# Kernel tuning notes

Measured on AMD Instinct MI355X. Metric: run time of the kernel, lower is better.

Reference implementation:

```python
import jax, jax.numpy as jnp
import numpy as np

H = 8        # num_heads
D = 768      # d_model
DH = D // H  # d_head = 96


def setup_inputs() -> dict:
    key = jax.random.key(0)
    ks = jax.random.split(key, 12)
    B, S = 4, 2048
    s_in = 1.0 / np.sqrt(D)
    s_cat = 1.0 / np.sqrt(D)
    return {
        "input_querys": jax.random.normal(ks[0], (B, S, D), jnp.float32),
        "input_key": jax.random.normal(ks[1], (B, S, D), jnp.float32),
        "input_values": jax.random.normal(ks[2], (B, S, D), jnp.float32),
        # per-head projection weights, stacked over the head axis
        "Wq": jax.random.normal(ks[3], (H, D, DH), jnp.float32) * s_in,
        "bq": jax.random.normal(ks[4], (H, DH), jnp.float32) * s_in,
        "Wk": jax.random.normal(ks[5], (H, D, DH), jnp.float32) * s_in,
        "bk": jax.random.normal(ks[6], (H, DH), jnp.float32) * s_in,
        "Wv": jax.random.normal(ks[7], (H, D, DH), jnp.float32) * s_in,
        "bv": jax.random.normal(ks[8], (H, DH), jnp.float32) * s_in,
        # output linear: (H*DH) -> D
        "Wo": jax.random.normal(ks[9], (H * DH, D), jnp.float32) * s_cat,
        "bo": jax.random.normal(ks[10], (D,), jnp.float32) * s_cat,
    }


def reference(input_querys, input_key, input_values, Wq, bq, Wk, bk, Wv, bv, Wo, bo):
    # Per-head linear projections (vectorized over the head axis)
    # q/k/v: [B,S,D] -> [B,H,S,DH]
    Q = jnp.einsum("bsd,hdk->bhsk", input_querys, Wq) + bq[None, :, None, :]
    K = jnp.einsum("bsd,hdk->bhsk", input_key, Wk) + bk[None, :, None, :]
    V = jnp.einsum("bsd,hdk->bhsk", input_values, Wv) + bv[None, :, None, :]

    scale = 1.0 / jnp.sqrt(jnp.asarray(DH, Q.dtype))
    scores = jnp.einsum("bhsk,bhtk->bhst", Q, K) * scale  # [B,H,S,S]
    attn = jax.nn.softmax(scores, axis=-1)
    out = jnp.einsum("bhst,bhtk->bhsk", attn, V)  # [B,H,S,DH]

    # concat heads (head-major order matches torch.cat over ModuleList)
    B, _, S, _ = out.shape
    cat = out.transpose(0, 2, 1, 3).reshape(B, S, H * DH)
    return cat @ Wo + bo
```

## Files before the change

kernel.cpp:

```cpp
#include <hip/hip_runtime.h>


typedef unsigned short u16;
typedef _Float16 h16;
typedef h16 h16x8 __attribute__((ext_vector_type(8)));
typedef __fp16 fp16x2 __attribute__((ext_vector_type(2)));
typedef unsigned short u16x8 __attribute__((ext_vector_type(8)));
typedef unsigned short u16x4 __attribute__((ext_vector_type(4)));
typedef float f32x4 __attribute__((ext_vector_type(4)));

__device__ __forceinline__ u16 f2h(float f) {
  union { h16 h; u16 u; } c; c.h = (h16)f; return c.u;
}

__device__ __forceinline__ void gll16(const void* g, void* l) {
  __builtin_amdgcn_global_load_lds(
      (const __attribute__((address_space(1))) void*)g,
      (__attribute__((address_space(3))) void*)l, 16, 0, 0);
}

__global__ __launch_bounds__(256) void prep_kernel(
    const float* __restrict__ Wq, const float* __restrict__ Wk,
    const float* __restrict__ Wv, const float* __restrict__ Wo,
    u16* __restrict__ WqT, u16* __restrict__ WkT,
    u16* __restrict__ WvT, u16* __restrict__ WoT)
{
  int idx = (blockIdx.x * 256 + threadIdx.x) * 8;
  int region = idx / 589824;
  int i = idx % 589824;
  int n = i / 768;
  int d = i % 768;
  u16x8 v;
  if (region == 3) {
    #pragma unroll
    for (int j = 0; j < 8; j++) v[j] = f2h(Wo[(size_t)(d + j) * 768 + n]);
    *(u16x8*)(&WoT[i]) = v;
  } else {
    int h = n / 96, kk = n % 96;
    const float* W = (region == 0) ? Wq : (region == 1) ? Wk : Wv;
    u16* T = (region == 0) ? WqT : (region == 1) ? WkT : WvT;
    #pragma unroll
    for (int j = 0; j < 8; j++) v[j] = f2h(W[(size_t)h * 73728 + (size_t)(d + j) * 96 + kk]);
    *(u16x8*)(&T[i]) = v;
  }
}

#define GK 768

__global__ __launch_bounds__(256) void gemm_qkv(
    const float* __restrict__ Xq, const float* __restrict__ Xk,
    const float* __restrict__ Xv, const u16* __restrict__ WT,
    const float* __restrict__ bq, const float* __restrict__ bk,
    const float* __restrict__ bv,
    u16* __restrict__ Q16, u16* __restrict__ K16, u16* __restrict__ VT)
{
  const int z = blockIdx.z;
  const float* A = (z == 0) ? Xq : (z == 1) ? Xk : Xv;
  const u16* BT = WT + (size_t)z * 589824;
  const float* bias = (z == 0) ? bq : (z == 1) ? bk : bv;

  __shared__ __align__(16) u16 As[128 * 32];
  __shared__ __align__(16) u16 Bs[64 * 32];
  const int tid = threadIdx.x;
  const int wave = tid >> 6;
  const int lane = tid & 63;
  const int quad = lane >> 4;
  const int l16 = lane & 15;
  const int m0 = blockIdx.y * 128;
  const int n0 = blockIdx.x * 64;

  f32x4 acc[2][4];
  #pragma unroll
  for (int i = 0; i < 2; i++)
    #pragma unroll
    for (int j = 0; j < 4; j++) acc[i][j] = (f32x4){0.f, 0.f, 0.f, 0.f};

  const int ar = tid >> 2;
  const int ac = (tid & 3) * 8;

  f32x4 pf[4];
  u16x8 pb;
  {
    pf[0] = *(const f32x4*)(&A[(size_t)(m0 + ar) * GK + ac]);
    pf[1] = *(const f32x4*)(&A[(size_t)(m0 + ar) * GK + ac + 4]);
    pf[2] = *(const f32x4*)(&A[(size_t)(m0 + 64 + ar) * GK + ac]);
    pf[3] = *(const f32x4*)(&A[(size_t)(m0 + 64 + ar) * GK + ac + 4]);
    pb = *(const u16x8*)(&BT[(size_t)(n0 + ar) * GK + ac]);
  }

  for (int kt = 0; kt < 24; kt++) {
    u16x8 h0, h1;
    #pragma unroll
    for (int j = 0; j < 4; j++) {
      h0[j] = f2h(pf[0][j]); h0[4 + j] = f2h(pf[1][j]);
      h1[j] = f2h(pf[2][j]); h1[4 + j] = f2h(pf[3][j]);
    }
    *(u16x8*)(&As[ar * 32 + ac]) = h0;
    *(u16x8*)(&As[(64 + ar) * 32 + ac]) = h1;
    *(u16x8*)(&Bs[ar * 32 + ac]) = pb;
    __syncthreads();

    if (kt + 1 < 24) {
      const int k0 = (kt + 1) * 32;
      pf[0] = *(const f32x4*)(&A[(size_t)(m0 + ar) * GK + k0 + ac]);
      pf[1] = *(const f32x4*)(&A[(size_t)(m0 + ar) * GK + k0 + ac + 4]);
      pf[2] = *(const f32x4*)(&A[(size_t)(m0 + 64 + ar) * GK + k0 + ac]);
      pf[3] = *(const f32x4*)(&A[(size_t)(m0 + 64 + ar) * GK + k0 + ac + 4]);
      pb = *(const u16x8*)(&BT[(size_t)(n0 + ar) * GK + k0 + ac]);
    }

    h16x8 af[2], bf[4];
    #pragma unroll
    for (int mf = 0; mf < 2; mf++)
      af[mf] = *(const h16x8*)(&As[(wave * 32 + mf * 16 + l16) * 32 + quad * 8]);
    #pragma unroll
    for (int nf = 0; nf < 4; nf++)
      bf[nf] = *(const h16x8*)(&Bs[(nf * 16 + l16) * 32 + quad * 8]);
    #pragma unroll
    for (int mf = 0; mf < 2; mf++)
      #pragma unroll
      for (int nf = 0; nf < 4; nf++)
        acc[mf][nf] = __builtin_amdgcn_mfma_f32_16x16x32_f16(af[mf], bf[nf], acc[mf][nf], 0, 0, 0);

    if (kt + 1 < 24) __syncthreads();
  }

  u16* Yr = (z == 0) ? Q16 : K16;
  #pragma unroll
  for (int nf = 0; nf < 4; nf++) {
    const int n = n0 + nf * 16 + l16;
    const float bv2 = bias[n];
    #pragma unroll
    for (int mf = 0; mf < 2; mf++) {
      const int m = m0 + wave * 32 + mf * 16 + quad * 4;
      if (z == 2) {
        const int b = m >> 11, s = m & 2047;
        u16x4 pk;
        #pragma unroll
        for (int r = 0; r < 4; r++) pk[r] = f2h(acc[mf][nf][r] + bv2);
        *(u16x4*)(&VT[(size_t)b * 768 * 2048 + (size_t)n * 2048 + s]) = pk;
      } else {
        #pragma unroll
        for (int r = 0; r < 4; r++)
          Yr[(size_t)(m + r) * GK + n] = f2h(acc[mf][nf][r] + bv2);
      }
    }
  }
}

__global__ __launch_bounds__(256) void gemm_o(
    const u16* __restrict__ A, const u16* __restrict__ BT,
    const float* __restrict__ bias, float* __restrict__ Y)
{
  __shared__ __align__(16) u16 As[128 * 32];
  __shared__ __align__(16) u16 Bs[64 * 32];
  const int tid = threadIdx.x;
  const int wave = tid >> 6;
  const int lane = tid & 63;
  const int quad = lane >> 4;
  const int l16 = lane & 15;
  const int m0 = blockIdx.y * 128;
  const int n0 = blockIdx.x * 64;

  f32x4 acc[2][4];
  #pragma unroll
  for (int i = 0; i < 2; i++)
    #pragma unroll
    for (int j = 0; j < 4; j++) acc[i][j] = (f32x4){0.f, 0.f, 0.f, 0.f};

  const int Lr = lane >> 2, Lc = (lane & 3) * 8;
  const u16* gA0 = A + (size_t)(m0 + wave * 32 + Lr) * GK + Lc;
  const u16* gA1 = gA0 + (size_t)16 * GK;
  const u16* gB  = BT + (size_t)(n0 + wave * 16 + Lr) * GK + Lc;
  u16* lA0 = &As[(wave * 32) * 32];
  u16* lA1 = &As[(wave * 32 + 16) * 32];
  u16* lB  = &Bs[(wave * 16) * 32];

  for (int kt = 0; kt < 24; kt++) {
    gll16(gA0, lA0);
    gll16(gA1, lA1);
    gll16(gB, lB);
    gA0 += 32; gA1 += 32; gB += 32;
    __syncthreads();

    h16x8 af[2], bf[4];
    #pragma unroll
    for (int mf = 0; mf < 2; mf++)
      af[mf] = *(const h16x8*)(&As[(wave * 32 + mf * 16 + l16) * 32 + quad * 8]);
    #pragma unroll
    for (int nf = 0; nf < 4; nf++)
      bf[nf] = *(const h16x8*)(&Bs[(nf * 16 + l16) * 32 + quad * 8]);
    #pragma unroll
    for (int mf = 0; mf < 2; mf++)
      #pragma unroll
      for (int nf = 0; nf < 4; nf++)
        acc[mf][nf] = __builtin_amdgcn_mfma_f32_16x16x32_f16(af[mf], bf[nf], acc[mf][nf], 0, 0, 0);
    __syncthreads();
  }

  #pragma unroll
  for (int nf = 0; nf < 4; nf++) {
    const int n = n0 + nf * 16 + l16;
    const float bv = bias[n];
    #pragma unroll
    for (int mf = 0; mf < 2; mf++) {
      const int m = m0 + wave * 32 + mf * 16 + quad * 4;
      #pragma unroll
      for (int r = 0; r < 4; r++)
        Y[(size_t)(m + r) * GK + n] = acc[mf][nf][r] + bv;
    }
  }
}

#define SEQ 2048
#define LQK 104
#define LVT 72
#define LPS 72

__global__ __launch_bounds__(256, 3) void attn_kernel(
    const u16* __restrict__ Q, const u16* __restrict__ K,
    const u16* __restrict__ VT, u16* __restrict__ O)
{
  __shared__ __align__(16) u16 Ks[64 * LQK];
  __shared__ __align__(16) u16 Vt[96 * LVT];
  __shared__ __align__(16) u16 Ps[4][32 * LPS];

  const int tid = threadIdx.x;
  const int wave = tid >> 6;
  const int lane = tid & 63;
  const int quad = lane >> 4;
  const int l16 = lane & 15;

  const int bh = blockIdx.y;
  const int b = bh >> 3, h = bh & 7;
  const int q0 = blockIdx.x * 128;

  const size_t batch_off = (size_t)b * SEQ * 768;
  const u16* Kg = K + batch_off + h * 96;
  const u16* Vg = VT + (size_t)b * 768 * 2048 + (size_t)(h * 96) * 2048;

  h16x8 qf[2][3];
  #pragma unroll
  for (int set = 0; set < 2; set++) {
    const u16* Qrow = Q + batch_off + (size_t)(q0 + wave * 32 + set * 16 + l16) * 768 + h * 96 + quad * 8;
    #pragma unroll
    for (int ks = 0; ks < 3; ks++) qf[set][ks] = *(const h16x8*)(&Qrow[ks * 32]);
  }

  int krr[3], kcc[3], vrr[3], vcc[3];
  #pragma unroll
  for (int j = 0; j < 3; j++) {
    int c = tid + j * 256;
    krr[j] = c / 12;  kcc[j] = (c % 12) * 8;
    vrr[j] = c >> 3;  vcc[j] = (c & 7) * 8;
  }

  f32x4 o[2][6];
  #pragma unroll
  for (int set = 0; set < 2; set++)
    #pragma unroll
    for (int i = 0; i < 6; i++) o[set][i] = (f32x4){0.f, 0.f, 0.f, 0.f};
  float m_raw[2] = {-1e30f, -1e30f}, lrow[2] = {0.f, 0.f};
  const float sc = 0.14724498f;

  u16* Pw = &Ps[wave][0];

  u16x8 kA[3], vA[3];
  #pragma unroll
  for (int j = 0; j < 3; j++) {
    kA[j] = *(const u16x8*)(&Kg[(size_t)krr[j] * 768 + kcc[j]]);
    vA[j] = *(const u16x8*)(&Vg[(size_t)vrr[j] * 2048 + vcc[j]]);
  }

  for (int kt = 0; kt < SEQ / 64; kt++) {
    #pragma unroll
    for (int j = 0; j < 3; j++) {
      *(u16x8*)(&Ks[krr[j] * LQK + kcc[j]]) = kA[j];
      *(u16x8*)(&Vt[vrr[j] * LVT + vcc[j]]) = vA[j];
    }
    __syncthreads();

    if (kt + 1 < SEQ / 64) {
      const u16* Kn = Kg + (size_t)(kt + 1) * 64 * 768;
      const u16* Vn = Vg + (size_t)(kt + 1) * 64;
      #pragma unroll
      for (int j = 0; j < 3; j++) {
        kA[j] = *(const u16x8*)(&Kn[(size_t)krr[j] * 768 + kcc[j]]);
        vA[j] = *(const u16x8*)(&Vn[(size_t)vrr[j] * 2048 + vcc[j]]);
      }
    }

    f32x4 s[2][4];
    #pragma unroll
    for (int set = 0; set < 2; set++)
      #pragma unroll
      for (int kf = 0; kf < 4; kf++) s[set][kf] = (f32x4){0.f, 0.f, 0.f, 0.f};
    #pragma unroll
    for (int ks = 0; ks < 3; ks++) {
      #pragma unroll
      for (int kf = 0; kf < 4; kf++) {
        h16x8 a = *(const h16x8*)(&Ks[(kf * 16 + l16) * LQK + ks * 32 + quad * 8]);
        s[0][kf] = __builtin_amdgcn_mfma_f32_16x16x32_f16(a, qf[0][ks], s[0][kf], 0, 0, 0);
        s[1][kf] = __builtin_amdgcn_mfma_f32_16x16x32_f16(a, qf[1][ks], s[1][kf], 0, 0, 0);
      }
    }

    #pragma unroll
    for (int set = 0; set < 2; set++) {
      float mx = s[set][0][0];
      #pragma unroll
      for (int kf = 0; kf < 4; kf++)
        #pragma unroll
        for (int r = 0; r < 4; r++) mx = fmaxf(mx, s[set][kf][r]);
      mx = fmaxf(mx, __shfl_xor(mx, 16));
      mx = fmaxf(mx, __shfl_xor(mx, 32));
      const float mold = m_raw[set];
      m_raw[set] = fmaxf(mold, mx);
      const float c0 = sc * m_raw[set];
      float ps = 0.f;
      #pragma unroll
      for (int kf = 0; kf < 4; kf++)
        #pragma unroll
        for (int r = 0; r < 4; r++) {
          float p = exp2f(fmaf(s[set][kf][r], sc, -c0));
          s[set][kf][r] = p;
          ps += p;
        }
      if (__any(m_raw[set] > mold)) {
        const float alpha = exp2f(sc * (mold - m_raw[set]));
        lrow[set] *= alpha;
        #pragma unroll
        for (int nfo = 0; nfo < 6; nfo++)
          #pragma unroll
          for (int r = 0; r < 4; r++) o[set][nfo][r] *= alpha;
      }
      lrow[set] += ps;

      #pragma unroll
      for (int kf = 0; kf < 4; kf++)
        #pragma unroll
        for (int rp = 0; rp < 4; rp += 2) {
          fp16x2 pk = __builtin_amdgcn_cvt_pkrtz(s[set][kf][rp], s[set][kf][rp + 1]);
          *(fp16x2*)(&Pw[(set * 16 + l16) * LPS + kf * 16 + quad * 4 + rp]) = pk;
        }
    }

    #pragma unroll
    for (int ks = 0; ks < 2; ks++) {
      h16x8 p0 = *(const h16x8*)(&Pw[l16 * LPS + ks * 32 + quad * 8]);
      h16x8 p1 = *(const h16x8*)(&Pw[(16 + l16) * LPS + ks * 32 + quad * 8]);
      #pragma unroll
      for (int nfo = 0; nfo < 6; nfo++) {
        h16x8 vfr = *(const h16x8*)(&Vt[(nfo * 16 + l16) * LVT + ks * 32 + quad * 8]);
        o[0][nfo] = __builtin_amdgcn_mfma_f32_16x16x32_f16(vfr, p0, o[0][nfo], 0, 0, 0);
        o[1][nfo] = __builtin_amdgcn_mfma_f32_16x16x32_f16(vfr, p1, o[1][nfo], 0, 0, 0);
      }
    }
    __syncthreads();
  }

  #pragma unroll
  for (int set = 0; set < 2; set++) {
    float l = lrow[set];
    l += __shfl_xor(l, 16);
    l += __shfl_xor(l, 32);
    const float inv = 1.0f / l;
    u16* Ob = O + batch_off + (size_t)(q0 + wave * 32 + set * 16 + l16) * 768 + h * 96;
    #pragma unroll
    for (int nfo = 0; nfo < 6; nfo++) {
      fp16x2 lo = __builtin_amdgcn_cvt_pkrtz(o[set][nfo][0] * inv, o[set][nfo][1] * inv);
      fp16x2 hi = __builtin_amdgcn_cvt_pkrtz(o[set][nfo][2] * inv, o[set][nfo][3] * inv);
      *(fp16x2*)(&Ob[nfo * 16 + quad * 4]) = lo;
      *(fp16x2*)(&Ob[nfo * 16 + quad * 4 + 2]) = hi;
    }
  }
}

extern "C" void kernel_launch(void* const* d_in, const int* in_sizes, int n_in,
                              void* d_out, int out_size, void* d_ws, size_t ws_size,
                              hipStream_t stream) {
  const float* Xq = (const float*)d_in[0];
  const float* Xk = (const float*)d_in[1];
  const float* Xv = (const float*)d_in[2];
  const float* Wq = (const float*)d_in[3];
  const float* bq = (const float*)d_in[4];
  const float* Wk = (const float*)d_in[5];
  const float* bk = (const float*)d_in[6];
  const float* Wv = (const float*)d_in[7];
  const float* bv = (const float*)d_in[8];
  const float* Wo = (const float*)d_in[9];
  const float* bo = (const float*)d_in[10];

  u16* wsu = (u16*)d_ws;
  u16* WT  = wsu;
  u16* WoT = wsu + 3 * 589824;
  u16* Q16 = wsu + 4 * 589824;

  u16* outu = (u16*)d_out;
  u16* VTb = outu;
  u16* K16 = outu + 6291456;

  u16* A16 = (u16*)d_in[0];

  prep_kernel<<<1152, 256, 0, stream>>>(Wq, Wk, Wv, Wo, WT, WT + 589824, WT + 2 * 589824, WoT);
  gemm_qkv<<<dim3(12, 64, 3), 256, 0, stream>>>(Xq, Xk, Xv, WT, bq, bk, bv, Q16, K16, VTb);
  attn_kernel<<<dim3(16, 32), 256, 0, stream>>>(Q16, K16, VTb, A16);
  gemm_o<<<dim3(12, 64), 256, 0, stream>>>(A16, WoT, bo, (float*)d_out);
}
```

Baseline: 355.9 us.

## Grow attention blocks to 512 threads and remap GEMM block IDs per XCD

The attention kernel now processes 256 query rows per block with 8 waves, so each K/V tile staged in shared memory is reused by twice as many waves. This halves the total K/V global traffic, at the cost of fewer blocks (256) on the device. Both GEMMs switch to a 1D grid with a block-ID swizzle that sends contiguous row tiles to the same XCD, to improve L2 locality. The grid is smaller and per-block register pressure may change under the new launch bounds.

```diff
diff --git a/kernel.cpp b/kernel.cpp
--- a/kernel.cpp
+++ b/kernel.cpp
@@ -54,7 +54,12 @@
     const float* __restrict__ bv,
     u16* __restrict__ Q16, u16* __restrict__ K16, u16* __restrict__ VT)
 {
-  const int z = blockIdx.z;
+  const int bid = blockIdx.x;
+  const int c = bid & 7, j = bid >> 3;
+  const int yz = c * 24 + j / 12;
+  const int xb = j % 12;
+  const int yb = yz & 63, z = yz >> 6;
+
   const float* A = (z == 0) ? Xq : (z == 1) ? Xk : Xv;
   const u16* BT = WT + (size_t)z * 589824;
   const float* bias = (z == 0) ? bq : (z == 1) ? bk : bv;
@@ -66,14 +71,14 @@
   const int lane = tid & 63;
   const int quad = lane >> 4;
   const int l16 = lane & 15;
-  const int m0 = blockIdx.y * 128;
-  const int n0 = blockIdx.x * 64;
+  const int m0 = yb * 128;
+  const int n0 = xb * 64;
 
   f32x4 acc[2][4];
   #pragma unroll
   for (int i = 0; i < 2; i++)
     #pragma unroll
-    for (int j = 0; j < 4; j++) acc[i][j] = (f32x4){0.f, 0.f, 0.f, 0.f};
+    for (int jj = 0; jj < 4; jj++) acc[i][jj] = (f32x4){0.f, 0.f, 0.f, 0.f};
 
   const int ar = tid >> 2;
   const int ac = (tid & 3) * 8;
@@ -91,9 +96,9 @@
   for (int kt = 0; kt < 24; kt++) {
     u16x8 h0, h1;
     #pragma unroll
-    for (int j = 0; j < 4; j++) {
-      h0[j] = f2h(pf[0][j]); h0[4 + j] = f2h(pf[1][j]);
-      h1[j] = f2h(pf[2][j]); h1[4 + j] = f2h(pf[3][j]);
+    for (int jj = 0; jj < 4; jj++) {
+      h0[jj] = f2h(pf[0][jj]); h0[4 + jj] = f2h(pf[1][jj]);
+      h1[jj] = f2h(pf[2][jj]); h1[4 + jj] = f2h(pf[3][jj]);
     }
     *(u16x8*)(&As[ar * 32 + ac]) = h0;
     *(u16x8*)(&As[(64 + ar) * 32 + ac]) = h1;
@@ -152,6 +157,11 @@
     const u16* __restrict__ A, const u16* __restrict__ BT,
     const float* __restrict__ bias, float* __restrict__ Y)
 {
+  const int bid = blockIdx.x;
+  const int c = bid & 7, j = bid >> 3;
+  const int yb = c * 8 + j / 12;
+  const int xb = j % 12;
+
   __shared__ __align__(16) u16 As[128 * 32];
   __shared__ __align__(16) u16 Bs[64 * 32];
   const int tid = threadIdx.x;
@@ -159,14 +169,14 @@
   const int lane = tid & 63;
   const int quad = lane >> 4;
   const int l16 = lane & 15;
-  const int m0 = blockIdx.y * 128;
-  const int n0 = blockIdx.x * 64;
+  const int m0 = yb * 128;
+  const int n0 = xb * 64;
 
   f32x4 acc[2][4];
   #pragma unroll
   for (int i = 0; i < 2; i++)
     #pragma unroll
-    for (int j = 0; j < 4; j++) acc[i][j] = (f32x4){0.f, 0.f, 0.f, 0.f};
+    for (int jj = 0; jj < 4; jj++) acc[i][jj] = (f32x4){0.f, 0.f, 0.f, 0.f};
 
   const int Lr = lane >> 2, Lc = (lane & 3) * 8;
   const u16* gA0 = A + (size_t)(m0 + wave * 32 + Lr) * GK + Lc;
@@ -217,13 +227,13 @@
 #define LVT 72
 #define LPS 72
 
-__global__ __launch_bounds__(256, 3) void attn_kernel(
+__global__ __launch_bounds__(512, 2) void attn_kernel(
     const u16* __restrict__ Q, const u16* __restrict__ K,
     const u16* __restrict__ VT, u16* __restrict__ O)
 {
   __shared__ __align__(16) u16 Ks[64 * LQK];
   __shared__ __align__(16) u16 Vt[96 * LVT];
-  __shared__ __align__(16) u16 Ps[4][32 * LPS];
+  __shared__ __align__(16) u16 Ps[8][32 * LPS];
 
   const int tid = threadIdx.x;
   const int wave = tid >> 6;
@@ -233,7 +243,7 @@
 
   const int bh = blockIdx.y;
   const int b = bh >> 3, h = bh & 7;
-  const int q0 = blockIdx.x * 128;
+  const int q0 = blockIdx.x * 256;
 
   const size_t batch_off = (size_t)b * SEQ * 768;
   const u16* Kg = K + batch_off + h * 96;
@@ -247,13 +257,11 @@
     for (int ks = 0; ks < 3; ks++) qf[set][ks] = *(const h16x8*)(&Qrow[ks * 32]);
   }
 
-  int krr[3], kcc[3], vrr[3], vcc[3];
-  #pragma unroll
-  for (int j = 0; j < 3; j++) {
-    int c = tid + j * 256;
-    krr[j] = c / 12;  kcc[j] = (c % 12) * 8;
-    vrr[j] = c >> 3;  vcc[j] = (c & 7) * 8;
-  }
+  const int kr0 = tid / 12, kc0 = (tid % 12) * 8;
+  const int kr1 = (tid + 512) / 12, kc1 = ((tid + 512) % 12) * 8;
+  const int vr0 = tid >> 3, vc0 = (tid & 7) * 8;
+  const int vr1 = (tid + 512) >> 3, vc1 = ((tid + 512) & 7) * 8;
+  const bool extra = tid < 256;
 
   f32x4 o[2][6];
   #pragma unroll
@@ -265,28 +273,31 @@
 
   u16* Pw = &Ps[wave][0];
 
-  u16x8 kA[3], vA[3];
-  #pragma unroll
-  for (int j = 0; j < 3; j++) {
-    kA[j] = *(const u16x8*)(&Kg[(size_t)krr[j] * 768 + kcc[j]]);
-    vA[j] = *(const u16x8*)(&Vg[(size_t)vrr[j] * 2048 + vcc[j]]);
+  u16x8 kA, kB, vA, vB;
+  kA = *(const u16x8*)(&Kg[(size_t)kr0 * 768 + kc0]);
+  vA = *(const u16x8*)(&Vg[(size_t)vr0 * 2048 + vc0]);
+  if (extra) {
+    kB = *(const u16x8*)(&Kg[(size_t)kr1 * 768 + kc1]);
+    vB = *(const u16x8*)(&Vg[(size_t)vr1 * 2048 + vc1]);
   }
 
   for (int kt = 0; kt < SEQ / 64; kt++) {
-    #pragma unroll
-    for (int j = 0; j < 3; j++) {
-      *(u16x8*)(&Ks[krr[j] * LQK + kcc[j]]) = kA[j];
-      *(u16x8*)(&Vt[vrr[j] * LVT + vcc[j]]) = vA[j];
+    *(u16x8*)(&Ks[kr0 * LQK + kc0]) = kA;
+    *(u16x8*)(&Vt[vr0 * LVT + vc0]) = vA;
+    if (extra) {
+      *(u16x8*)(&Ks[kr1 * LQK + kc1]) = kB;
+      *(u16x8*)(&Vt[vr1 * LVT + vc1]) = vB;
     }
     __syncthreads();
 
     if (kt + 1 < SEQ / 64) {
       const u16* Kn = Kg + (size_t)(kt + 1) * 64 * 768;
       const u16* Vn = Vg + (size_t)(kt + 1) * 64;
-      #pragma unroll
-      for (int j = 0; j < 3; j++) {
-        kA[j] = *(const u16x8*)(&Kn[(size_t)krr[j] * 768 + kcc[j]]);
-        vA[j] = *(const u16x8*)(&Vn[(size_t)vrr[j] * 2048 + vcc[j]]);
+      kA = *(const u16x8*)(&Kn[(size_t)kr0 * 768 + kc0]);
+      vA = *(const u16x8*)(&Vn[(size_t)vr0 * 2048 + vc0]);
+      if (extra) {
+        kB = *(const u16x8*)(&Kn[(size_t)kr1 * 768 + kc1]);
+        vB = *(const u16x8*)(&Vn[(size_t)vr1 * 2048 + vc1]);
       }
     }
 
@@ -403,7 +414,7 @@
   u16* A16 = (u16*)d_in[0];
 
   prep_kernel<<<1152, 256, 0, stream>>>(Wq, Wk, Wv, Wo, WT, WT + 589824, WT + 2 * 589824, WoT);
-  gemm_qkv<<<dim3(12, 64, 3), 256, 0, stream>>>(Xq, Xk, Xv, WT, bq, bk, bv, Q16, K16, VTb);
-  attn_kernel<<<dim3(16, 32), 256, 0, stream>>>(Q16, K16, VTb, A16);
-  gemm_o<<<dim3(12, 64), 256, 0, stream>>>(A16, WoT, bo, (float*)d_out);
-}
+  gemm_qkv<<<2304, 256, 0, stream>>>(Xq, Xk, Xv, WT, bq, bk, bv, Q16, K16, VTb);
+  attn_kernel<<<dim3(8, 32), 512, 0, stream>>>(Q16, K16, VTb, A16);
+  gemm_o<<<768, 256, 0, stream>>>(A16, WoT, bo, (float*)d_out);
+}
```

Result: faster. 328.6 us (-7.7%).
